# Kernel tuning notes

Measured on AMD Instinct MI355X. Metric: run time of the kernel, lower is better.

The kernel has to match this reference:

```python
import jax, jax.numpy as jnp
import numpy as np

D = 768           # input_dim == slot_dim
H, DH = 8, 64     # encoder attention heads / head dim (x-transformers defaults)
INNER = 4 * D     # ff_mult=4 GLU inner dim
EPS = 1e-8
N_ITERS = 3
SCALE = D ** -0.5


def _ln(x, g, b):
    m = jnp.mean(x, axis=-1, keepdims=True)
    v = jnp.var(x, axis=-1, keepdims=True)
    return (x - m) / jnp.sqrt(v + 1e-5) * g + b


def setup_inputs() -> dict:
    key = jax.random.key(0)
    ks = jax.random.split(key, 16)
    w = lambda i, shape, s=0.02: jax.random.normal(ks[i], shape, jnp.float32) * s
    return dict(
        x=jax.random.normal(ks[0], (32, 1024, D), jnp.float32),
        noise=jax.random.normal(ks[1], (32, 16, D), jnp.float32),
        init_mu=jax.random.normal(ks[2], (D,), jnp.float32),
        init_log_sigma=w(3, (D,), 0.05),
        Wk=w(4, (D, D)), Wv=w(5, (D, D)), Wq=w(6, (D, D)),
        ni_g=jnp.ones(D), ni_b=jnp.zeros(D),       # norm_input
        ns_g=jnp.ones(D), ns_b=jnp.zeros(D),       # norm_slots
        nica_g=jnp.ones(D), nica_b=jnp.zeros(D),   # norm_ica
        ln1_g=jnp.ones(D), ln1_b=jnp.zeros(D),     # encoder attn pre-norm
        Wq_a=w(7, (D, H * DH)), Wk_a=w(8, (D, H * DH)),
        Wv_a=w(9, (D, H * DH)), Wo_a=w(10, (H * DH, D)),
        ln2_g=jnp.ones(D), ln2_b=jnp.zeros(D),     # encoder ff pre-norm
        W1=w(11, (D, 2 * INNER)), W2=w(12, (INNER, D)),
        lnf_g=jnp.ones(D), lnf_b=jnp.zeros(D),     # encoder final norm
    )


def _inv_cross_attn(q, k, v):
    # softmax over the SLOT axis (dim i), then renormalize over keys j
    dots = jnp.einsum('bid,bjd->bij', q, k) * SCALE
    attn = jax.nn.softmax(dots, axis=1) + EPS
    attn = attn / jnp.sum(attn, axis=-1, keepdims=True)
    updates = jnp.einsum('bjd,bij->bid', v, attn)
    return updates, attn


def _encoder(h, ln1_g, ln1_b, Wq_a, Wk_a, Wv_a, Wo_a, ln2_g, ln2_b, W1, W2, lnf_g, lnf_b):
    b, n, _ = h.shape
    a = _ln(h, ln1_g, ln1_b)
    q = (a @ Wq_a).reshape(b, n, H, DH)
    k = (a @ Wk_a).reshape(b, n, H, DH)
    v = (a @ Wv_a).reshape(b, n, H, DH)
    scores = jnp.einsum('bihd,bjhd->bhij', q, k) * (DH ** -0.5)
    p = jax.nn.softmax(scores, axis=-1)
    o = jnp.einsum('bhij,bjhd->bihd', p, v).reshape(b, n, H * DH)
    h = h + o @ Wo_a
    f = _ln(h, ln2_g, ln2_b)
    u, g = jnp.split(f @ W1, 2, axis=-1)
    h = h + (u * jax.nn.silu(g)) @ W2
    return _ln(h, lnf_g, lnf_b)


def reference(x, noise, init_mu, init_log_sigma, Wk, Wv, Wq,
              ni_g, ni_b, ns_g, ns_b, nica_g, nica_b,
              ln1_g, ln1_b, Wq_a, Wk_a, Wv_a, Wo_a,
              ln2_g, ln2_b, W1, W2, lnf_g, lnf_b):
    xn = _ln(x, ni_g, ni_b)
    k = xn @ Wk
    v = xn @ Wv
    slots = init_mu + jnp.exp(init_log_sigma) * noise  # [b, n_slots, d]

    def step(slots):
        q = _ln(slots, ns_g, ns_b) @ Wq
        updates, attn = _inv_cross_attn(q, k, v)
        slots = _ln(slots + updates, nica_g, nica_b)
        slots = _encoder(slots, ln1_g, ln1_b, Wq_a, Wk_a, Wv_a, Wo_a,
                         ln2_g, ln2_b, W1, W2, lnf_g, lnf_b)
        return slots, attn

    for _ in range(N_ITERS):
        slots, _ = step(slots)
    slots, attn = step(slots)
    attn_map = jnp.transpose(attn, (0, 2, 1))  # b n hw -> b hw n
    return slots, attn_map
```

## Files before the change

kernel.cpp:

```cpp
#include <hip/hip_runtime.h>
#include <hip/hip_bf16.h>
#include <stdint.h>

typedef _Float16 f16;
typedef __attribute__((ext_vector_type(8))) _Float16 f16x8;
typedef __attribute__((ext_vector_type(4))) _Float16 f16x4;
typedef __attribute__((ext_vector_type(4))) float f32x4;

#define GLOBAL_AS __attribute__((address_space(1)))
#define LDS_AS __attribute__((address_space(3)))

#define D_DIM 768
#define NTOK 1024
#define NSLOT 16
#define NB 32
#define NTOT (NB*NTOK)
#define HDIM 512
#define INNER 3072
#define SCALE_D 0.03608439182435161f
#define SCALE_H 0.125f

template<int OUT>
__global__ __launch_bounds__(256) void mgemm64_k(
    const f16* __restrict__ A, const f16* __restrict__ Bt,
    void* __restrict__ Cout, int M, int N, int K, int Kc)
{
  __shared__ __align__(16) f16 As[64*128];
  __shared__ __align__(16) f16 Bs[64*128];
  const int tid = threadIdx.x;
  const int lane = tid & 63;
  const int wave = tid >> 6;
  const int m0 = blockIdx.x*64, n0 = blockIdx.y*64;
  const int kbeg = blockIdx.z * Kc;
  const int wm = (wave>>1)*32, wn = (wave&1)*32;
  const int quad = lane>>4, l16 = lane&15;

  const int sr = tid>>2;
  const int sc = (tid&3)*8;
  const f16* gA = A  + (size_t)(m0+sr)*K + kbeg + sc;
  const f16* gB = Bt + (size_t)(n0+sr)*K + kbeg + sc;
  LDS_AS f16* lA = (LDS_AS f16*)&As[(size_t)tid*8];
  LDS_AS f16* lB = (LDS_AS f16*)&Bs[(size_t)tid*8];

  const f16* fA0 = &As[(wm + l16)*32 + quad*8];
  const f16* fB0 = &Bs[(wn + l16)*32 + quad*8];

  f32x4 acc[2][2] = {};

  for (int k0 = 0; k0 < Kc; k0 += 128){
    #pragma unroll
    for (int p=0;p<4;++p){
      __builtin_amdgcn_global_load_lds((const GLOBAL_AS void*)(gA + k0 + p*32),
                                       (LDS_AS void*)(lA + (size_t)p*2048), 16, 0, 0);
      __builtin_amdgcn_global_load_lds((const GLOBAL_AS void*)(gB + k0 + p*32),
                                       (LDS_AS void*)(lB + (size_t)p*2048), 16, 0, 0);
    }
    __syncthreads();
    #pragma unroll
    for (int p=0;p<4;++p){
      f16x8 a0 = *(const f16x8*)(fA0 + p*2048);
      f16x8 a1 = *(const f16x8*)(fA0 + p*2048 + 16*32);
      f16x8 b0 = *(const f16x8*)(fB0 + p*2048);
      f16x8 b1 = *(const f16x8*)(fB0 + p*2048 + 16*32);
      acc[0][0] = __builtin_amdgcn_mfma_f32_16x16x32_f16(a0,b0,acc[0][0],0,0,0);
      acc[0][1] = __builtin_amdgcn_mfma_f32_16x16x32_f16(a0,b1,acc[0][1],0,0,0);
      acc[1][0] = __builtin_amdgcn_mfma_f32_16x16x32_f16(a1,b0,acc[1][0],0,0,0);
      acc[1][1] = __builtin_amdgcn_mfma_f32_16x16x32_f16(a1,b1,acc[1][1],0,0,0);
    }
    __syncthreads();
  }
  #pragma unroll
  for (int mt=0;mt<2;++mt){
    #pragma unroll
    for (int nt=0;nt<2;++nt){
      int gm = m0 + wm + mt*16 + quad*4;
      int gn = n0 + wn + nt*16 + l16;
      #pragma unroll
      for (int r=0;r<4;++r){
        float c = acc[mt][nt][r];
        size_t idx = (size_t)(gm+r)*N + gn;
        if (OUT==0)      ((float*)Cout)[idx] = c;
        else if (OUT==1) ((f16*)Cout)[idx] = (f16)c;
        else             atomicAdd(&((float*)Cout)[idx], c);
      }
    }
  }
}

__global__ __launch_bounds__(256) void w1glu_k(
    const f16* __restrict__ A, const f16* __restrict__ W1T,
    f16* __restrict__ act, int M)
{
  __shared__ __align__(16) f16 As[64*128];
  __shared__ __align__(16) f16 Bu[64*128];
  __shared__ __align__(16) f16 Bg[64*128];
  const int K = 768;
  const int tid = threadIdx.x;
  const int lane = tid & 63;
  const int wave = tid >> 6;
  const int m0 = blockIdx.x*64, n0 = blockIdx.y*64;
  const int wm = (wave>>1)*32, wn = (wave&1)*32;
  const int quad = lane>>4, l16 = lane&15;

  const int sr = tid>>2;
  const int sc = (tid&3)*8;
  const f16* gA  = A   + (size_t)(m0+sr)*K + sc;
  const f16* gBu = W1T + (size_t)(n0+sr)*K + sc;
  const f16* gBg = W1T + (size_t)(3072+n0+sr)*K + sc;
  LDS_AS f16* lA  = (LDS_AS f16*)&As[(size_t)tid*8];
  LDS_AS f16* lBu = (LDS_AS f16*)&Bu[(size_t)tid*8];
  LDS_AS f16* lBg = (LDS_AS f16*)&Bg[(size_t)tid*8];

  const f16* fA0 = &As[(wm + l16)*32 + quad*8];
  const f16* fU0 = &Bu[(wn + l16)*32 + quad*8];
  const f16* fG0 = &Bg[(wn + l16)*32 + quad*8];

  f32x4 accU[2][2] = {};
  f32x4 accG[2][2] = {};

  for (int k0 = 0; k0 < K; k0 += 128){
    #pragma unroll
    for (int p=0;p<4;++p){
      __builtin_amdgcn_global_load_lds((const GLOBAL_AS void*)(gA  + k0 + p*32),
                                       (LDS_AS void*)(lA  + (size_t)p*2048), 16, 0, 0);
      __builtin_amdgcn_global_load_lds((const GLOBAL_AS void*)(gBu + k0 + p*32),
                                       (LDS_AS void*)(lBu + (size_t)p*2048), 16, 0, 0);
      __builtin_amdgcn_global_load_lds((const GLOBAL_AS void*)(gBg + k0 + p*32),
                                       (LDS_AS void*)(lBg + (size_t)p*2048), 16, 0, 0);
    }
    __syncthreads();
    #pragma unroll
    for (int p=0;p<4;++p){
      f16x8 a0 = *(const f16x8*)(fA0 + p*2048);
      f16x8 a1 = *(const f16x8*)(fA0 + p*2048 + 16*32);
      f16x8 u0 = *(const f16x8*)(fU0 + p*2048);
      f16x8 u1 = *(const f16x8*)(fU0 + p*2048 + 16*32);
      f16x8 g0 = *(const f16x8*)(fG0 + p*2048);
      f16x8 g1 = *(const f16x8*)(fG0 + p*2048 + 16*32);
      accU[0][0] = __builtin_amdgcn_mfma_f32_16x16x32_f16(a0,u0,accU[0][0],0,0,0);
      accU[0][1] = __builtin_amdgcn_mfma_f32_16x16x32_f16(a0,u1,accU[0][1],0,0,0);
      accU[1][0] = __builtin_amdgcn_mfma_f32_16x16x32_f16(a1,u0,accU[1][0],0,0,0);
      accU[1][1] = __builtin_amdgcn_mfma_f32_16x16x32_f16(a1,u1,accU[1][1],0,0,0);
      accG[0][0] = __builtin_amdgcn_mfma_f32_16x16x32_f16(a0,g0,accG[0][0],0,0,0);
      accG[0][1] = __builtin_amdgcn_mfma_f32_16x16x32_f16(a0,g1,accG[0][1],0,0,0);
      accG[1][0] = __builtin_amdgcn_mfma_f32_16x16x32_f16(a1,g0,accG[1][0],0,0,0);
      accG[1][1] = __builtin_amdgcn_mfma_f32_16x16x32_f16(a1,g1,accG[1][1],0,0,0);
    }
    __syncthreads();
  }
  #pragma unroll
  for (int mt=0;mt<2;++mt){
    #pragma unroll
    for (int nt=0;nt<2;++nt){
      int gm = m0 + wm + mt*16 + quad*4;
      int gn = n0 + wn + nt*16 + l16;
      #pragma unroll
      for (int r=0;r<4;++r){
        float u = accU[mt][nt][r];
        float g = accG[mt][nt][r];
        float sg = g / (1.0f + __expf(-g));
        act[(size_t)(gm+r)*INNER + gn] = (f16)(u*sg);
      }
    }
  }
}

__global__ __launch_bounds__(256) void dots_k(
    const f16* __restrict__ Q,
    const f16* __restrict__ Xn,
    f16* __restrict__ attn,
    float* __restrict__ rsPart)
{
  __shared__ __align__(16) f16 qf[16*768];
  __shared__ __align__(16) f16 ks[64*128];
  __shared__ float rpart[4][16];
  const int b = blockIdx.x, jt = blockIdx.y;
  const int tid = threadIdx.x;
  const int lane = tid & 63;
  const int w = tid >> 6;
  const int quad = lane>>4, l16 = lane&15;

  #pragma unroll
  for (int c=0;c<6;++c){
    int p = c*256 + tid;
    int ki = p >> 6, qd = (p >> 4) & 3, rw = p & 15;
    f16x8 v = *(const f16x8*)(Q + ((size_t)(b*NSLOT+rw))*D_DIM + ki*32 + qd*8);
    *(f16x8*)&qf[(size_t)p*8] = v;
  }

  const f16* gK = Xn + ((size_t)(b*NTOK + jt*64 + (tid>>2)))*D_DIM + (tid&3)*8;
  LDS_AS f16* lK = (LDS_AS f16*)&ks[(size_t)tid*8];

  f32x4 acc = {};
  for (int it=0; it<6; ++it){
    #pragma unroll
    for (int p=0;p<4;++p)
      __builtin_amdgcn_global_load_lds((const GLOBAL_AS void*)(gK + it*128 + p*32),
                                       (LDS_AS void*)(lK + (size_t)p*2048), 16, 0, 0);
    __syncthreads();
    #pragma unroll
    for (int p=0;p<4;++p){
      f16x8 a  = *(const f16x8*)&qf[(((size_t)(it*4+p)*4 + quad)*16 + l16)*8];
      f16x8 bf = *(const f16x8*)&ks[(size_t)p*2048 + (w*16+l16)*32 + quad*8];
      acc = __builtin_amdgcn_mfma_f32_16x16x32_f16(a, bf, acc, 0, 0, 0);
    }
    __syncthreads();
  }

  float v0 = acc[0]*SCALE_D, v1 = acc[1]*SCALE_D, v2 = acc[2]*SCALE_D, v3 = acc[3]*SCALE_D;
  float mx = fmaxf(fmaxf(v0,v1), fmaxf(v2,v3));
  mx = fmaxf(mx, __shfl_xor(mx, 16));
  mx = fmaxf(mx, __shfl_xor(mx, 32));
  float e0 = __expf(v0-mx), e1 = __expf(v1-mx), e2 = __expf(v2-mx), e3 = __expf(v3-mx);
  float s = e0+e1+e2+e3;
  s += __shfl_xor(s, 16);
  s += __shfl_xor(s, 32);
  float inv = 1.0f/s;
  float a0 = e0*inv + 1e-8f, a1 = e1*inv + 1e-8f, a2 = e2*inv + 1e-8f, a3 = e3*inv + 1e-8f;

  int jcol = jt*64 + w*16 + l16;
  int ibase = b*NSLOT + quad*4;
  attn[(size_t)(ibase+0)*NTOK + jcol] = (f16)a0;
  attn[(size_t)(ibase+1)*NTOK + jcol] = (f16)a1;
  attn[(size_t)(ibase+2)*NTOK + jcol] = (f16)a2;
  attn[(size_t)(ibase+3)*NTOK + jcol] = (f16)a3;

  float t0=a0, t1=a1, t2=a2, t3=a3;
  #pragma unroll
  for (int m=1;m<16;m<<=1){
    t0 += __shfl_xor(t0, m);
    t1 += __shfl_xor(t1, m);
    t2 += __shfl_xor(t2, m);
    t3 += __shfl_xor(t3, m);
  }
  if (l16 == 0){
    rpart[w][quad*4+0] = t0;
    rpart[w][quad*4+1] = t1;
    rpart[w][quad*4+2] = t2;
    rpart[w][quad*4+3] = t3;
  }
  __syncthreads();
  if (tid < 16){
    float ss = rpart[0][tid] + rpart[1][tid] + rpart[2][tid] + rpart[3][tid];
    rsPart[(size_t)((b*16 + jt)<<4) + tid] = ss;
  }
}

__global__ __launch_bounds__(256) void attnv_k(
    const f16* __restrict__ attn,
    const float* __restrict__ rsPart,
    const f16* __restrict__ XnT,
    f16* __restrict__ t_out)
{
  __shared__ __align__(16) f16 Asl[16*128];
  __shared__ __align__(16) f16 Bsl[64*128];
  __shared__ float rsum[16];
  const int b = blockIdx.x, d0 = blockIdx.y*64;
  const int tid = threadIdx.x;
  const int lane = tid & 63;
  const int w = tid >> 6;
  const int quad = lane>>4, l16 = lane&15;

  if (tid < 16){
    float s = 0.f;
    #pragma unroll
    for (int jt=0;jt<16;++jt) s += rsPart[(size_t)((b*16 + jt)<<4) + tid];
    rsum[tid] = s;
  }

  const int pa = tid>>6, ta = tid&63;
  const f16* gA = attn + ((size_t)(b*NSLOT + (ta>>2)))*NTOK + pa*32 + (ta&3)*8;
  LDS_AS f16* lA = (LDS_AS f16*)&Asl[(size_t)pa*512 + ta*8];
  const f16* gB = XnT + ((size_t)(d0 + (tid>>2)))*NTOT + b*NTOK + (tid&3)*8;
  LDS_AS f16* lB = (LDS_AS f16*)&Bsl[(size_t)tid*8];

  f32x4 acc = {};
  for (int it=0; it<8; ++it){
    __builtin_amdgcn_global_load_lds((const GLOBAL_AS void*)(gA + it*128),
                                     (LDS_AS void*)lA, 16, 0, 0);
    #pragma unroll
    for (int p=0;p<4;++p)
      __builtin_amdgcn_global_load_lds((const GLOBAL_AS void*)(gB + it*128 + p*32),
                                       (LDS_AS void*)(lB + (size_t)p*2048), 16, 0, 0);
    __syncthreads();
    #pragma unroll
    for (int p=0;p<4;++p){
      f16x8 a  = *(const f16x8*)&Asl[(size_t)p*512 + l16*32 + quad*8];
      f16x8 bf = *(const f16x8*)&Bsl[(size_t)p*2048 + (w*16+l16)*32 + quad*8];
      acc = __builtin_amdgcn_mfma_f32_16x16x32_f16(a, bf, acc, 0, 0, 0);
    }
    __syncthreads();
  }
  int dcol = d0 + w*16 + l16;
  #pragma unroll
  for (int r=0;r<4;++r){
    int i = quad*4 + r;
    t_out[(size_t)(b*NSLOT + i)*D_DIM + dcol] = (f16)(acc[r] / rsum[i]);
  }
}

template<bool ADD, int OUT>
__global__ __launch_bounds__(256) void ln_k(
    const float* __restrict__ X, const float* __restrict__ X2,
    const float* __restrict__ g, const float* __restrict__ bb,
    void* __restrict__ out)
{
  __shared__ float rs[256], rss[256];
  const int row = blockIdx.x, tid = threadIdx.x;
  const float* x = X + (size_t)row*D_DIM;
  float vals[3]; float s=0.f, ss=0.f;
  #pragma unroll
  for (int t=0;t<3;++t){
    int c = tid + t*256;
    float v = x[c];
    if (ADD) v += X2[(size_t)row*D_DIM + c];
    vals[t]=v; s+=v; ss+=v*v;
  }
  rs[tid]=s; rss[tid]=ss; __syncthreads();
  for (int off=128; off>0; off>>=1){
    if (tid<off){ rs[tid]+=rs[tid+off]; rss[tid]+=rss[tid+off]; }
    __syncthreads();
  }
  float mean = rs[0]*(1.0f/768.0f);
  float var  = rss[0]*(1.0f/768.0f) - mean*mean;
  float inv  = rsqrtf(var + 1e-5f);
  #pragma unroll
  for (int t=0;t<3;++t){
    int c = tid + t*256;
    float y = (vals[t]-mean)*inv*g[c] + bb[c];
    if (OUT==1) ((f16*)out)[(size_t)row*D_DIM + c] = (f16)y;
    else        ((float*)out)[(size_t)row*D_DIM + c] = y;
  }
}

template<bool ADD>
__global__ __launch_bounds__(256) void lnln_k(
    const float* __restrict__ X, const float* __restrict__ X2,
    const float* __restrict__ g1, const float* __restrict__ b1,
    const float* __restrict__ g2, const float* __restrict__ b2,
    float* __restrict__ out1, f16* __restrict__ out2)
{
  __shared__ float rs[256], rss[256];
  const int row = blockIdx.x, tid = threadIdx.x;
  const float* x = X + (size_t)row*D_DIM;
  float vals[3]; float s=0.f, ss=0.f;
  #pragma unroll
  for (int t=0;t<3;++t){
    int c = tid + t*256;
    float v = x[c];
    if (ADD) v += X2[(size_t)row*D_DIM + c];
    vals[t]=v; s+=v; ss+=v*v;
  }
  rs[tid]=s; rss[tid]=ss; __syncthreads();
  for (int off=128; off>0; off>>=1){
    if (tid<off){ rs[tid]+=rs[tid+off]; rss[tid]+=rss[tid+off]; }
    __syncthreads();
  }
  float mean = rs[0]*(1.0f/768.0f);
  float var  = rss[0]*(1.0f/768.0f) - mean*mean;
  float inv  = rsqrtf(var + 1e-5f);
  float y[3]; float s2=0.f, ss2=0.f;
  #pragma unroll
  for (int t=0;t<3;++t){
    int c = tid + t*256;
    float yy = (vals[t]-mean)*inv*g1[c] + b1[c];
    y[t]=yy; s2+=yy; ss2+=yy*yy;
    out1[(size_t)row*D_DIM + c] = yy;
  }
  __syncthreads();
  rs[tid]=s2; rss[tid]=ss2; __syncthreads();
  for (int off=128; off>0; off>>=1){
    if (tid<off){ rs[tid]+=rs[tid+off]; rss[tid]+=rss[tid+off]; }
    __syncthreads();
  }
  float mean2 = rs[0]*(1.0f/768.0f);
  float var2  = rss[0]*(1.0f/768.0f) - mean2*mean2;
  float inv2  = rsqrtf(var2 + 1e-5f);
  #pragma unroll
  for (int t=0;t<3;++t){
    int c = tid + t*256;
    out2[(size_t)row*D_DIM + c] = (f16)((y[t]-mean2)*inv2*g2[c] + b2[c]);
  }
}

__global__ __launch_bounds__(256) void slots_init_k(
    const float* __restrict__ noise, const float* __restrict__ mu,
    const float* __restrict__ ls, float* __restrict__ slots)
{
  int idx = blockIdx.x*256 + threadIdx.x;
  int d = idx % D_DIM;
  slots[idx] = mu[d] + expf(ls[d]) * noise[idx];
}

__global__ __launch_bounds__(256) void encattn_k(
    const f16* __restrict__ QA, const f16* __restrict__ KA,
    const f16* __restrict__ VA, int QSTR,
    f16* __restrict__ O)
{
  __shared__ float qs[16][68], ks[16][68], vs[16][68], ps[16][20];
  const int b = blockIdx.x, h = blockIdx.y;
  const int tid = threadIdx.x;
  {
    int i = tid>>4, dd=(tid&15)*4;
    size_t base = ((size_t)(b*NSLOT+i))*QSTR + h*64 + dd;
    f16x4 uq = *(const f16x4*)(QA + base);
    f16x4 uk = *(const f16x4*)(KA + base);
    f16x4 uv = *(const f16x4*)(VA + base);
    float4 fq = { (float)uq.x, (float)uq.y, (float)uq.z, (float)uq.w };
    float4 fk = { (float)uk.x, (float)uk.y, (float)uk.z, (float)uk.w };
    float4 fv = { (float)uv.x, (float)uv.y, (float)uv.z, (float)uv.w };
    *(float4*)&qs[i][dd]=fq; *(float4*)&ks[i][dd]=fk; *(float4*)&vs[i][dd]=fv;
  }
  __syncthreads();
  {
    int i = tid>>4, j = tid&15;
    float s=0.f;
    #pragma unroll 8
    for (int d=0; d<64; ++d) s += qs[i][d]*ks[j][d];
    ps[i][j] = s*SCALE_H;
  }
  __syncthreads();
  if (tid < 16){
    int i = tid;
    float mx=-1e30f;
    #pragma unroll
    for (int j=0;j<16;++j) mx = fmaxf(mx, ps[i][j]);
    float sm=0.f;
    #pragma unroll
    for (int j=0;j<16;++j){ float e=__expf(ps[i][j]-mx); ps[i][j]=e; sm+=e; }
    float inv=1.0f/sm;
    #pragma unroll
    for (int j=0;j<16;++j) ps[i][j]*=inv;
  }
  __syncthreads();
  {
    int i = tid>>4, dq=(tid&15)*4;
    float a0=0,a1=0,a2=0,a3=0;
    #pragma unroll
    for (int j=0;j<16;++j){
      float p = ps[i][j];
      a0+=p*vs[j][dq+0]; a1+=p*vs[j][dq+1]; a2+=p*vs[j][dq+2]; a3+=p*vs[j][dq+3];
    }
    size_t base = ((size_t)(b*NSLOT+i))*HDIM + h*64 + dq;
    O[base+0]=(f16)a0; O[base+1]=(f16)a1; O[base+2]=(f16)a2; O[base+3]=(f16)a3;
  }
}

__global__ __launch_bounds__(256) void cast_t_k(
    const float* __restrict__ in, f16* __restrict__ out, int R, int C)
{
  __shared__ float t[32][33];
  int r0 = blockIdx.x*32, c0 = blockIdx.y*32;
  int tr = threadIdx.x & 31, g8 = threadIdx.x >> 5;
  #pragma unroll
  for (int s=0;s<4;++s){
    int r = g8*4 + s;
    t[r][tr] = in[(size_t)(r0+r)*C + c0+tr];
  }
  __syncthreads();
  #pragma unroll
  for (int s=0;s<4;++s){
    int c = g8*4+s;
    out[(size_t)(c0+c)*R + r0+tr] = (f16)t[tr][c];
  }
}

__global__ __launch_bounds__(256) void cast_k(
    const float* __restrict__ in, f16* __restrict__ out, int n)
{
  int i = blockIdx.x*256 + threadIdx.x;
  if (i < n) out[i] = (f16)in[i];
}

__global__ __launch_bounds__(256) void transp_k(
    const f16* __restrict__ in, f16* __restrict__ out, int R, int C)
{
  __shared__ f16 T[64][72];
  const int m0 = blockIdx.x*64, d0 = blockIdx.y*64;
  const int tid = threadIdx.x;
  {
    int r = tid>>2, c = (tid&3)*16;
    const f16* p = in + (size_t)(m0+r)*C + d0 + c;
    *(f16x8*)&T[r][c]   = *(const f16x8*)p;
    *(f16x8*)&T[r][c+8] = *(const f16x8*)(p+8);
  }
  __syncthreads();
  {
    int dd = tid>>2, mq = (tid&3)*16;
    f16 v[16];
    #pragma unroll
    for (int e=0;e<16;++e) v[e] = T[mq+e][dd];
    f16* p = out + (size_t)(d0+dd)*R + m0 + mq;
    *(f16x8*)p     = *(f16x8*)&v[0];
    *(f16x8*)(p+8) = *(f16x8*)&v[8];
  }
}

__global__ __launch_bounds__(256) void rsfin_k(
    const float* __restrict__ rsPart, float* __restrict__ rowsum)
{
  int idx = blockIdx.x*256 + threadIdx.x;
  if (idx < 512){
    int b = idx>>4, i = idx&15;
    float s = 0.f;
    #pragma unroll
    for (int jt=0;jt<16;++jt) s += rsPart[(size_t)((b*16+jt)<<4) + i];
    rowsum[idx] = s;
  }
}

__global__ __launch_bounds__(256) void attnout_k(
    const f16* __restrict__ attn, const float* __restrict__ rowsum,
    float* __restrict__ out)
{
  int idx = blockIdx.x*256 + threadIdx.x;
  int i = idx & 15;
  int j = (idx >> 4) & 1023;
  int b = idx >> 14;
  out[idx] = (float)attn[((size_t)b*NSLOT+i)*NTOK + j] / rowsum[b*NSLOT + i];
}

extern "C" void kernel_launch(void* const* d_in, const int* in_sizes, int n_in,
                              void* d_out, int out_size, void* d_ws, size_t ws_size,
                              hipStream_t stream) {
  const float* x        = (const float*)d_in[0];
  const float* noise    = (const float*)d_in[1];
  const float* init_mu  = (const float*)d_in[2];
  const float* init_ls  = (const float*)d_in[3];
  const float* Wk       = (const float*)d_in[4];
  const float* Wv       = (const float*)d_in[5];
  const float* Wq       = (const float*)d_in[6];
  const float* ni_g     = (const float*)d_in[7];
  const float* ni_b     = (const float*)d_in[8];
  const float* ns_g     = (const float*)d_in[9];
  const float* ns_b     = (const float*)d_in[10];
  const float* nica_g   = (const float*)d_in[11];
  const float* nica_b   = (const float*)d_in[12];
  const float* ln1_g    = (const float*)d_in[13];
  const float* ln1_b    = (const float*)d_in[14];
  const float* Wq_a     = (const float*)d_in[15];
  const float* Wk_a     = (const float*)d_in[16];
  const float* Wv_a     = (const float*)d_in[17];
  const float* Wo_a     = (const float*)d_in[18];
  const float* ln2_g    = (const float*)d_in[19];
  const float* ln2_b    = (const float*)d_in[20];
  const float* W1       = (const float*)d_in[21];
  const float* W2       = (const float*)d_in[22];
  const float* lnf_g    = (const float*)d_in[23];
  const float* lnf_b    = (const float*)d_in[24];

  char* w = (char*)d_ws;
  size_t off = 0;
  auto alloc = [&](size_t bytes)->char*{
    char* p = w + off; off += (bytes + 255) & ~(size_t)255; return p;
  };
  f16* xn_h  = (f16*)alloc((size_t)NTOT*D_DIM*2);
  f16* xnT_h = (f16*)alloc((size_t)D_DIM*NTOT*2);
  f16* Wkf   = (f16*)alloc((size_t)768*768*2);
  f16* Wqf   = (f16*)alloc((size_t)768*768*2);
  f16* BtQK  = (f16*)alloc((size_t)768*768*2);
  f16* WvT   = (f16*)alloc((size_t)768*768*2);
  f16* WqkvT = (f16*)alloc((size_t)1536*768*2);
  f16* WoaT  = (f16*)alloc((size_t)768*512*2);
  f16* W1T   = (f16*)alloc((size_t)6144*768*2);
  f16* W2T   = (f16*)alloc((size_t)768*3072*2);
  float* slots = (float*)alloc(512*768*4);
  float* hbuf  = (float*)alloc(512*768*4);
  float* upd   = (float*)alloc(512*768*4);
  f16* tmp_h  = (f16*)alloc(512*768*2);
  f16* tmp2_h = (f16*)alloc(512*768*2);
  f16* q_h    = (f16*)alloc(512*768*2);
  f16* t_h    = (f16*)alloc(512*768*2);
  f16* qkv_h  = (f16*)alloc((size_t)512*1536*2);
  f16* o_h    = (f16*)alloc(512*512*2);
  f16* act_h  = (f16*)alloc((size_t)512*3072*2);
  f16* attn_h = (f16*)alloc((size_t)NB*NSLOT*NTOK*2);
  float* rsPart = (float*)alloc((size_t)32*16*16*4);
  float* rowsum = (float*)alloc(512*4);

  auto castT = [&](const float* src, f16* dst, int R, int C){
    cast_t_k<<<dim3(R/32, C/32), 256, 0, stream>>>(src, dst, R, C);
  };
  cast_k<<<768*768/256, 256, 0, stream>>>(Wk, Wkf, 768*768);
  cast_k<<<768*768/256, 256, 0, stream>>>(Wq, Wqf, 768*768);
  castT(Wv,   WvT,             768, 768);
  castT(Wq_a, WqkvT,             768, 512);
  castT(Wk_a, WqkvT + 512*768,   768, 512);
  castT(Wv_a, WqkvT + 1024*768,  768, 512);
  castT(Wo_a, WoaT,            512, 768);
  castT(W1,   W1T,             768, 6144);
  castT(W2,   W2T,             3072, 768);

  mgemm64_k<1><<<dim3(12, 12, 1), 256, 0, stream>>>(Wkf, Wqf, BtQK, 768, 768, 768, 768);

  ln_k<false,1><<<NTOT, 256, 0, stream>>>(x, nullptr, ni_g, ni_b, xn_h);
  transp_k<<<dim3(NTOT/64, D_DIM/64), 256, 0, stream>>>(xn_h, xnT_h, NTOT, D_DIM);

  slots_init_k<<<512*768/256, 256, 0, stream>>>(noise, init_mu, init_ls, slots);
  ln_k<false,1><<<512, 256, 0, stream>>>(slots, nullptr, ns_g, ns_b, tmp2_h);

  for (int it=0; it<4; ++it){
    mgemm64_k<1><<<dim3(8, 12, 1), 256, 0, stream>>>(tmp2_h, BtQK, q_h, 512, 768, 768, 768);
    dots_k<<<dim3(NB, 16), 256, 0, stream>>>(q_h, xn_h, attn_h, rsPart);
    attnv_k<<<dim3(NB, 12), 256, 0, stream>>>(attn_h, rsPart, xnT_h, t_h);
    mgemm64_k<0><<<dim3(8, 12, 1), 256, 0, stream>>>(t_h, WvT, upd, 512, 768, 768, 768);
    lnln_k<true><<<512, 256, 0, stream>>>(slots, upd, nica_g, nica_b, ln1_g, ln1_b, hbuf, tmp_h);
    mgemm64_k<1><<<dim3(8, 24, 1), 256, 0, stream>>>(tmp_h, WqkvT, qkv_h, 512, 1536, 768, 768);
    encattn_k<<<dim3(NB, 8), 256, 0, stream>>>(qkv_h, qkv_h + 512, qkv_h + 1024, 1536, o_h);
    mgemm64_k<2><<<dim3(8, 12, 2), 256, 0, stream>>>(o_h, WoaT, hbuf, 512, 768, 512, 256);
    ln_k<false,1><<<512, 256, 0, stream>>>(hbuf, nullptr, ln2_g, ln2_b, tmp_h);
    w1glu_k<<<dim3(8, 48), 256, 0, stream>>>(tmp_h, W1T, act_h, 512);
    mgemm64_k<2><<<dim3(8, 12, 4), 256, 0, stream>>>(act_h, W2T, hbuf, 512, 768, 3072, 768);
    lnln_k<false><<<512, 256, 0, stream>>>(hbuf, nullptr, lnf_g, lnf_b, ns_g, ns_b, slots, tmp2_h);
  }

  hipMemcpyAsync(d_out, slots, (size_t)512*768*4, hipMemcpyDeviceToDevice, stream);
  rsfin_k<<<2, 256, 0, stream>>>(rsPart, rowsum);
  attnout_k<<<NB*NTOK*NSLOT/256, 256, 0, stream>>>(attn_h, rowsum, (float*)d_out + 512*768);
}
```

Measured before the change: 664.6 us.

## Fuse Wv and Wo projections into attention kernels, wave-level layernorms, merged prep

Folds the V-projection GEMM into attnv_k and the Wo projection into the encoder attention kernel, accumulating each into a residual buffer with atomics so the separate GEMMs and intermediate buffers go away. The residual buffer is pre-seeded with the slots so the slot residual add comes for free. LayerNorm kernels are rewritten to handle one row per wave using float4 loads and shuffle reductions. The weight cast and transpose launches are merged into one prep kernel, and the rowsum finalisation is folded into attnout. The atomic accumulation adds contention and makes summation order nondeterministic.

```diff
diff --git a/kernel.cpp b/kernel.cpp
--- a/kernel.cpp
+++ b/kernel.cpp
@@ -79,9 +79,8 @@
       for (int r=0;r<4;++r){
         float c = acc[mt][nt][r];
         size_t idx = (size_t)(gm+r)*N + gn;
-        if (OUT==0)      ((float*)Cout)[idx] = c;
-        else if (OUT==1) ((f16*)Cout)[idx] = (f16)c;
-        else             atomicAdd(&((float*)Cout)[idx], c);
+        if (OUT==1) ((f16*)Cout)[idx] = (f16)c;
+        else        atomicAdd(&((float*)Cout)[idx], c);
       }
     }
   }
@@ -250,11 +249,13 @@
     const f16* __restrict__ attn,
     const float* __restrict__ rsPart,
     const f16* __restrict__ XnT,
-    f16* __restrict__ t_out)
+    const f16* __restrict__ WvT,
+    float* __restrict__ accb)
 {
   __shared__ __align__(16) f16 Asl[16*128];
   __shared__ __align__(16) f16 Bsl[64*128];
   __shared__ float rsum[16];
+  __shared__ __align__(16) f16 tl[16][80];
   const int b = blockIdx.x, d0 = blockIdx.y*64;
   const int tid = threadIdx.x;
   const int lane = tid & 63;
@@ -291,113 +292,166 @@
     }
     __syncthreads();
   }
-  int dcol = d0 + w*16 + l16;
-  #pragma unroll
-  for (int r=0;r<4;++r){
-    int i = quad*4 + r;
-    t_out[(size_t)(b*NSLOT + i)*D_DIM + dcol] = (f16)(acc[r] / rsum[i]);
-  }
-}
-
-template<bool ADD, int OUT>
-__global__ __launch_bounds__(256) void ln_k(
-    const float* __restrict__ X, const float* __restrict__ X2,
+  const int dloc = w*16 + l16;
+  #pragma unroll
+  for (int r=0;r<4;++r)
+    tl[quad*4+r][dloc] = (f16)(acc[r] / rsum[quad*4+r]);
+  __syncthreads();
+  f16x8 af0 = *(const f16x8*)&tl[l16][quad*8];
+  f16x8 af1 = *(const f16x8*)&tl[l16][32 + quad*8];
+  const f16* bp = WvT + (size_t)l16*D_DIM + d0 + quad*8;
+  float* up = accb + (size_t)(b*NSLOT + quad*4)*D_DIM + l16;
+  #pragma unroll
+  for (int j=0;j<12;++j){
+    int n0 = (w*12 + j)*16;
+    f16x8 b0 = *(const f16x8*)(bp + (size_t)n0*D_DIM);
+    f16x8 b1 = *(const f16x8*)(bp + (size_t)n0*D_DIM + 32);
+    f32x4 c = {};
+    c = __builtin_amdgcn_mfma_f32_16x16x32_f16(af0, b0, c, 0,0,0);
+    c = __builtin_amdgcn_mfma_f32_16x16x32_f16(af1, b1, c, 0,0,0);
+    #pragma unroll
+    for (int r=0;r<4;++r) atomicAdd(up + (size_t)r*D_DIM + n0, c[r]);
+  }
+}
+
+__global__ __launch_bounds__(256) void lnw_k(
+    const float* __restrict__ X,
     const float* __restrict__ g, const float* __restrict__ bb,
-    void* __restrict__ out)
-{
-  __shared__ float rs[256], rss[256];
-  const int row = blockIdx.x, tid = threadIdx.x;
-  const float* x = X + (size_t)row*D_DIM;
-  float vals[3]; float s=0.f, ss=0.f;
+    f16* __restrict__ out)
+{
+  const int lane = threadIdx.x & 63;
+  const size_t row = (size_t)blockIdx.x*4 + (threadIdx.x>>6);
+  const float* x = X + row*D_DIM;
+  float4 v[3]; float s=0.f, ss=0.f;
   #pragma unroll
   for (int t=0;t<3;++t){
-    int c = tid + t*256;
-    float v = x[c];
-    if (ADD) v += X2[(size_t)row*D_DIM + c];
-    vals[t]=v; s+=v; ss+=v*v;
-  }
-  rs[tid]=s; rss[tid]=ss; __syncthreads();
-  for (int off=128; off>0; off>>=1){
-    if (tid<off){ rs[tid]+=rs[tid+off]; rss[tid]+=rss[tid+off]; }
-    __syncthreads();
-  }
-  float mean = rs[0]*(1.0f/768.0f);
-  float var  = rss[0]*(1.0f/768.0f) - mean*mean;
-  float inv  = rsqrtf(var + 1e-5f);
+    v[t] = *(const float4*)(x + lane*4 + t*256);
+    s  += v[t].x+v[t].y+v[t].z+v[t].w;
+    ss += v[t].x*v[t].x+v[t].y*v[t].y+v[t].z*v[t].z+v[t].w*v[t].w;
+  }
+  #pragma unroll
+  for (int m=1;m<64;m<<=1){ s += __shfl_xor(s,m); ss += __shfl_xor(ss,m); }
+  float mean = s*(1.0f/768.0f);
+  float inv  = rsqrtf(ss*(1.0f/768.0f) - mean*mean + 1e-5f);
   #pragma unroll
   for (int t=0;t<3;++t){
-    int c = tid + t*256;
-    float y = (vals[t]-mean)*inv*g[c] + bb[c];
-    if (OUT==1) ((f16*)out)[(size_t)row*D_DIM + c] = (f16)y;
-    else        ((float*)out)[(size_t)row*D_DIM + c] = y;
-  }
-}
-
-template<bool ADD>
-__global__ __launch_bounds__(256) void lnln_k(
-    const float* __restrict__ X, const float* __restrict__ X2,
+    int c0 = lane*4 + t*256;
+    float4 gg = *(const float4*)(g + c0);
+    float4 bv = *(const float4*)(bb + c0);
+    f16x4 h4;
+    h4.x = (f16)((v[t].x-mean)*inv*gg.x + bv.x);
+    h4.y = (f16)((v[t].y-mean)*inv*gg.y + bv.y);
+    h4.z = (f16)((v[t].z-mean)*inv*gg.z + bv.z);
+    h4.w = (f16)((v[t].w-mean)*inv*gg.w + bv.w);
+    *(f16x4*)(out + row*D_DIM + c0) = h4;
+  }
+}
+
+template<bool WACC>
+__global__ __launch_bounds__(256) void lnlnw_k(
+    const float* __restrict__ X,
     const float* __restrict__ g1, const float* __restrict__ b1,
     const float* __restrict__ g2, const float* __restrict__ b2,
-    float* __restrict__ out1, f16* __restrict__ out2)
-{
-  __shared__ float rs[256], rss[256];
-  const int row = blockIdx.x, tid = threadIdx.x;
-  const float* x = X + (size_t)row*D_DIM;
-  float vals[3]; float s=0.f, ss=0.f;
+    float* __restrict__ out1, f16* __restrict__ out2, float* __restrict__ acc)
+{
+  const int lane = threadIdx.x & 63;
+  const size_t row = (size_t)blockIdx.x*4 + (threadIdx.x>>6);
+  const float* x = X + row*D_DIM;
+  float4 v[3]; float s=0.f, ss=0.f;
   #pragma unroll
   for (int t=0;t<3;++t){
-    int c = tid + t*256;
-    float v = x[c];
-    if (ADD) v += X2[(size_t)row*D_DIM + c];
-    vals[t]=v; s+=v; ss+=v*v;
-  }
-  rs[tid]=s; rss[tid]=ss; __syncthreads();
-  for (int off=128; off>0; off>>=1){
-    if (tid<off){ rs[tid]+=rs[tid+off]; rss[tid]+=rss[tid+off]; }
-    __syncthreads();
-  }
-  float mean = rs[0]*(1.0f/768.0f);
-  float var  = rss[0]*(1.0f/768.0f) - mean*mean;
-  float inv  = rsqrtf(var + 1e-5f);
-  float y[3]; float s2=0.f, ss2=0.f;
+    v[t] = *(const float4*)(x + lane*4 + t*256);
+    s  += v[t].x+v[t].y+v[t].z+v[t].w;
+    ss += v[t].x*v[t].x+v[t].y*v[t].y+v[t].z*v[t].z+v[t].w*v[t].w;
+  }
+  #pragma unroll
+  for (int m=1;m<64;m<<=1){ s += __shfl_xor(s,m); ss += __shfl_xor(ss,m); }
+  float mean = s*(1.0f/768.0f);
+  float inv  = rsqrtf(ss*(1.0f/768.0f) - mean*mean + 1e-5f);
+  float y[3][4]; float s2=0.f, ss2=0.f;
   #pragma unroll
   for (int t=0;t<3;++t){
-    int c = tid + t*256;
-    float yy = (vals[t]-mean)*inv*g1[c] + b1[c];
-    y[t]=yy; s2+=yy; ss2+=yy*yy;
-    out1[(size_t)row*D_DIM + c] = yy;
-  }
-  __syncthreads();
-  rs[tid]=s2; rss[tid]=ss2; __syncthreads();
-  for (int off=128; off>0; off>>=1){
-    if (tid<off){ rs[tid]+=rs[tid+off]; rss[tid]+=rss[tid+off]; }
-    __syncthreads();
-  }
-  float mean2 = rs[0]*(1.0f/768.0f);
-  float var2  = rss[0]*(1.0f/768.0f) - mean2*mean2;
-  float inv2  = rsqrtf(var2 + 1e-5f);
+    int c0 = lane*4 + t*256;
+    float4 gg = *(const float4*)(g1 + c0);
+    float4 bv = *(const float4*)(b1 + c0);
+    y[t][0] = (v[t].x-mean)*inv*gg.x + bv.x;
+    y[t][1] = (v[t].y-mean)*inv*gg.y + bv.y;
+    y[t][2] = (v[t].z-mean)*inv*gg.z + bv.z;
+    y[t][3] = (v[t].w-mean)*inv*gg.w + bv.w;
+    float4 o = { y[t][0], y[t][1], y[t][2], y[t][3] };
+    *(float4*)(out1 + row*D_DIM + c0) = o;
+    if (WACC) *(float4*)(acc + row*D_DIM + c0) = o;
+    s2  += y[t][0]+y[t][1]+y[t][2]+y[t][3];
+    ss2 += y[t][0]*y[t][0]+y[t][1]*y[t][1]+y[t][2]*y[t][2]+y[t][3]*y[t][3];
+  }
+  #pragma unroll
+  for (int m=1;m<64;m<<=1){ s2 += __shfl_xor(s2,m); ss2 += __shfl_xor(ss2,m); }
+  float mean2 = s2*(1.0f/768.0f);
+  float inv2  = rsqrtf(ss2*(1.0f/768.0f) - mean2*mean2 + 1e-5f);
   #pragma unroll
   for (int t=0;t<3;++t){
-    int c = tid + t*256;
-    out2[(size_t)row*D_DIM + c] = (f16)((y[t]-mean2)*inv2*g2[c] + b2[c]);
-  }
-}
-
-__global__ __launch_bounds__(256) void slots_init_k(
+    int c0 = lane*4 + t*256;
+    float4 gg = *(const float4*)(g2 + c0);
+    float4 bv = *(const float4*)(b2 + c0);
+    f16x4 h4;
+    h4.x = (f16)((y[t][0]-mean2)*inv2*gg.x + bv.x);
+    h4.y = (f16)((y[t][1]-mean2)*inv2*gg.y + bv.y);
+    h4.z = (f16)((y[t][2]-mean2)*inv2*gg.z + bv.z);
+    h4.w = (f16)((y[t][3]-mean2)*inv2*gg.w + bv.w);
+    *(f16x4*)(out2 + row*D_DIM + c0) = h4;
+  }
+}
+
+__global__ __launch_bounds__(256) void slotsinit_k(
     const float* __restrict__ noise, const float* __restrict__ mu,
-    const float* __restrict__ ls, float* __restrict__ slots)
-{
-  int idx = blockIdx.x*256 + threadIdx.x;
-  int d = idx % D_DIM;
-  slots[idx] = mu[d] + expf(ls[d]) * noise[idx];
-}
-
-__global__ __launch_bounds__(256) void encattn_k(
+    const float* __restrict__ ls,
+    const float* __restrict__ nsg, const float* __restrict__ nsb,
+    float* __restrict__ slots, float* __restrict__ accb, f16* __restrict__ tmp2)
+{
+  const int lane = threadIdx.x & 63;
+  const size_t row = (size_t)blockIdx.x*4 + (threadIdx.x>>6);
+  float4 v[3]; float s=0.f, ss=0.f;
+  #pragma unroll
+  for (int t=0;t<3;++t){
+    int c0 = lane*4 + t*256;
+    float4 nz = *(const float4*)(noise + row*D_DIM + c0);
+    float4 m4 = *(const float4*)(mu + c0);
+    float4 l4 = *(const float4*)(ls + c0);
+    v[t].x = m4.x + __expf(l4.x)*nz.x;
+    v[t].y = m4.y + __expf(l4.y)*nz.y;
+    v[t].z = m4.z + __expf(l4.z)*nz.z;
+    v[t].w = m4.w + __expf(l4.w)*nz.w;
+    *(float4*)(slots + row*D_DIM + c0) = v[t];
+    *(float4*)(accb  + row*D_DIM + c0) = v[t];
+    s  += v[t].x+v[t].y+v[t].z+v[t].w;
+    ss += v[t].x*v[t].x+v[t].y*v[t].y+v[t].z*v[t].z+v[t].w*v[t].w;
+  }
+  #pragma unroll
+  for (int m=1;m<64;m<<=1){ s += __shfl_xor(s,m); ss += __shfl_xor(ss,m); }
+  float mean = s*(1.0f/768.0f);
+  float inv  = rsqrtf(ss*(1.0f/768.0f) - mean*mean + 1e-5f);
+  #pragma unroll
+  for (int t=0;t<3;++t){
+    int c0 = lane*4 + t*256;
+    float4 gg = *(const float4*)(nsg + c0);
+    float4 bv = *(const float4*)(nsb + c0);
+    f16x4 h4;
+    h4.x = (f16)((v[t].x-mean)*inv*gg.x + bv.x);
+    h4.y = (f16)((v[t].y-mean)*inv*gg.y + bv.y);
+    h4.z = (f16)((v[t].z-mean)*inv*gg.z + bv.z);
+    h4.w = (f16)((v[t].w-mean)*inv*gg.w + bv.w);
+    *(f16x4*)(tmp2 + row*D_DIM + c0) = h4;
+  }
+}
+
+__global__ __launch_bounds__(256) void encwo_k(
     const f16* __restrict__ QA, const f16* __restrict__ KA,
     const f16* __restrict__ VA, int QSTR,
-    f16* __restrict__ O)
+    const f16* __restrict__ WoT,
+    float* __restrict__ hb)
 {
   __shared__ float qs[16][68], ks[16][68], vs[16][68], ps[16][20];
+  __shared__ __align__(16) f16 ol[16][80];
   const int b = blockIdx.x, h = blockIdx.y;
   const int tid = threadIdx.x;
   {
@@ -441,35 +495,26 @@
       float p = ps[i][j];
       a0+=p*vs[j][dq+0]; a1+=p*vs[j][dq+1]; a2+=p*vs[j][dq+2]; a3+=p*vs[j][dq+3];
     }
-    size_t base = ((size_t)(b*NSLOT+i))*HDIM + h*64 + dq;
-    O[base+0]=(f16)a0; O[base+1]=(f16)a1; O[base+2]=(f16)a2; O[base+3]=(f16)a3;
-  }
-}
-
-__global__ __launch_bounds__(256) void cast_t_k(
-    const float* __restrict__ in, f16* __restrict__ out, int R, int C)
-{
-  __shared__ float t[32][33];
-  int r0 = blockIdx.x*32, c0 = blockIdx.y*32;
-  int tr = threadIdx.x & 31, g8 = threadIdx.x >> 5;
-  #pragma unroll
-  for (int s=0;s<4;++s){
-    int r = g8*4 + s;
-    t[r][tr] = in[(size_t)(r0+r)*C + c0+tr];
-  }
-  __syncthreads();
-  #pragma unroll
-  for (int s=0;s<4;++s){
-    int c = g8*4+s;
-    out[(size_t)(c0+c)*R + r0+tr] = (f16)t[tr][c];
-  }
-}
-
-__global__ __launch_bounds__(256) void cast_k(
-    const float* __restrict__ in, f16* __restrict__ out, int n)
-{
-  int i = blockIdx.x*256 + threadIdx.x;
-  if (i < n) out[i] = (f16)in[i];
+    f16x4 o4 = { (f16)a0, (f16)a1, (f16)a2, (f16)a3 };
+    *(f16x4*)&ol[i][dq] = o4;
+  }
+  __syncthreads();
+  const int lane = tid & 63, w = tid>>6, quad = lane>>4, l16 = lane&15;
+  f16x8 af0 = *(const f16x8*)&ol[l16][quad*8];
+  f16x8 af1 = *(const f16x8*)&ol[l16][32 + quad*8];
+  const f16* bp = WoT + (size_t)l16*HDIM + h*64 + quad*8;
+  float* hp = hb + (size_t)(b*NSLOT + quad*4)*D_DIM + l16;
+  #pragma unroll
+  for (int j=0;j<12;++j){
+    int n0 = (w*12 + j)*16;
+    f16x8 b0 = *(const f16x8*)(bp + (size_t)n0*HDIM);
+    f16x8 b1 = *(const f16x8*)(bp + (size_t)n0*HDIM + 32);
+    f32x4 c = {};
+    c = __builtin_amdgcn_mfma_f32_16x16x32_f16(af0, b0, c, 0,0,0);
+    c = __builtin_amdgcn_mfma_f32_16x16x32_f16(af1, b1, c, 0,0,0);
+    #pragma unroll
+    for (int r=0;r<4;++r) atomicAdd(hp + (size_t)r*D_DIM + n0, c[r]);
+  }
 }
 
 __global__ __launch_bounds__(256) void transp_k(
@@ -496,28 +541,70 @@
   }
 }
 
-__global__ __launch_bounds__(256) void rsfin_k(
-    const float* __restrict__ rsPart, float* __restrict__ rowsum)
-{
-  int idx = blockIdx.x*256 + threadIdx.x;
-  if (idx < 512){
-    int b = idx>>4, i = idx&15;
+__global__ __launch_bounds__(256) void prep_k(
+    const float* __restrict__ Wv,   const float* __restrict__ Wq_a,
+    const float* __restrict__ Wk_a, const float* __restrict__ Wv_a,
+    const float* __restrict__ Wo_a, const float* __restrict__ W1,
+    const float* __restrict__ W2,   const float* __restrict__ Wk,
+    const float* __restrict__ Wq,
+    f16* __restrict__ WvT, f16* __restrict__ WqkvT, f16* __restrict__ WoaT,
+    f16* __restrict__ W1T, f16* __restrict__ W2T,
+    f16* __restrict__ Wkf, f16* __restrict__ Wqf)
+{
+  __shared__ float t[32][33];
+  int bid = blockIdx.x;
+  const float* src; f16* dst; int R, C; bool tr = true;
+  if      (bid < 576)  {              src=Wv;   dst=WvT;             R=768;  C=768; }
+  else if (bid < 960)  { bid-=576;    src=Wq_a; dst=WqkvT;           R=768;  C=512; }
+  else if (bid < 1344) { bid-=960;    src=Wk_a; dst=WqkvT+512*768;   R=768;  C=512; }
+  else if (bid < 1728) { bid-=1344;   src=Wv_a; dst=WqkvT+1024*768;  R=768;  C=512; }
+  else if (bid < 2112) { bid-=1728;   src=Wo_a; dst=WoaT;            R=512;  C=768; }
+  else if (bid < 6720) { bid-=2112;   src=W1;   dst=W1T;             R=768;  C=6144; }
+  else if (bid < 9024) { bid-=6720;   src=W2;   dst=W2T;             R=3072; C=768; }
+  else if (bid < 9600) { bid-=9024;   src=Wk;   dst=Wkf;             R=768;  C=768; tr=false; }
+  else                 { bid-=9600;   src=Wq;   dst=Wqf;             R=768;  C=768; tr=false; }
+  const int tpr = C/32;
+  const int r0 = (bid / tpr)*32, c0 = (bid % tpr)*32;
+  const int lc = threadIdx.x & 31, g8 = threadIdx.x >> 5;
+  if (tr){
+    #pragma unroll
+    for (int s=0;s<4;++s){
+      int r = g8*4 + s;
+      t[r][lc] = src[(size_t)(r0+r)*C + c0+lc];
+    }
+    __syncthreads();
+    #pragma unroll
+    for (int s=0;s<4;++s){
+      int c = g8*4 + s;
+      dst[(size_t)(c0+c)*R + r0+lc] = (f16)t[lc][c];
+    }
+  } else {
+    #pragma unroll
+    for (int s=0;s<4;++s){
+      int r = g8*4 + s;
+      dst[(size_t)(r0+r)*C + c0+lc] = (f16)src[(size_t)(r0+r)*C + c0+lc];
+    }
+  }
+}
+
+__global__ __launch_bounds__(256) void attnout_k(
+    const f16* __restrict__ attn, const float* __restrict__ rsPart,
+    float* __restrict__ out)
+{
+  __shared__ float rsum[16];
+  const int bid = blockIdx.x, tid = threadIdx.x;
+  const int b = bid >> 6;
+  if (tid < 16){
     float s = 0.f;
     #pragma unroll
-    for (int jt=0;jt<16;++jt) s += rsPart[(size_t)((b*16+jt)<<4) + i];
-    rowsum[idx] = s;
-  }
-}
-
-__global__ __launch_bounds__(256) void attnout_k(
-    const f16* __restrict__ attn, const float* __restrict__ rowsum,
-    float* __restrict__ out)
-{
-  int idx = blockIdx.x*256 + threadIdx.x;
+    for (int jt=0;jt<16;++jt) s += rsPart[(size_t)((b*16+jt)<<4) + tid];
+    rsum[tid] = s;
+  }
+  __syncthreads();
+  int idx = bid*256 + tid;
   int i = idx & 15;
   int j = (idx >> 4) & 1023;
-  int b = idx >> 14;
-  out[idx] = (float)attn[((size_t)b*NSLOT+i)*NTOK + j] / rowsum[b*NSLOT + i];
+  out[idx] = (float)attn[((size_t)(b*NSLOT)+i)*NTOK + j] / rsum[i];
 }
 
 extern "C" void kernel_launch(void* const* d_in, const int* in_sizes, int n_in,
@@ -566,55 +653,42 @@
   f16* W2T   = (f16*)alloc((size_t)768*3072*2);
   float* slots = (float*)alloc(512*768*4);
   float* hbuf  = (float*)alloc(512*768*4);
-  float* upd   = (float*)alloc(512*768*4);
+  float* accb  = (float*)alloc(512*768*4);
   f16* tmp_h  = (f16*)alloc(512*768*2);
   f16* tmp2_h = (f16*)alloc(512*768*2);
   f16* q_h    = (f16*)alloc(512*768*2);
-  f16* t_h    = (f16*)alloc(512*768*2);
   f16* qkv_h  = (f16*)alloc((size_t)512*1536*2);
-  f16* o_h    = (f16*)alloc(512*512*2);
   f16* act_h  = (f16*)alloc((size_t)512*3072*2);
   f16* attn_h = (f16*)alloc((size_t)NB*NSLOT*NTOK*2);
   float* rsPart = (float*)alloc((size_t)32*16*16*4);
-  float* rowsum = (float*)alloc(512*4);
-
-  auto castT = [&](const float* src, f16* dst, int R, int C){
-    cast_t_k<<<dim3(R/32, C/32), 256, 0, stream>>>(src, dst, R, C);
-  };
-  cast_k<<<768*768/256, 256, 0, stream>>>(Wk, Wkf, 768*768);
-  cast_k<<<768*768/256, 256, 0, stream>>>(Wq, Wqf, 768*768);
-  castT(Wv,   WvT,             768, 768);
-  castT(Wq_a, WqkvT,             768, 512);
-  castT(Wk_a, WqkvT + 512*768,   768, 512);
-  castT(Wv_a, WqkvT + 1024*768,  768, 512);
-  castT(Wo_a, WoaT,            512, 768);
-  castT(W1,   W1T,             768, 6144);
-  castT(W2,   W2T,             3072, 768);
+
+  prep_k<<<10176, 256, 0, stream>>>(Wv, Wq_a, Wk_a, Wv_a, Wo_a, W1, W2, Wk, Wq,
+                                    WvT, WqkvT, WoaT, W1T, W2T, Wkf, Wqf);
 
   mgemm64_k<1><<<dim3(12, 12, 1), 256, 0, stream>>>(Wkf, Wqf, BtQK, 768, 768, 768, 768);
 
-  ln_k<false,1><<<NTOT, 256, 0, stream>>>(x, nullptr, ni_g, ni_b, xn_h);
+  lnw_k<<<NTOT/4, 256, 0, stream>>>(x, ni_g, ni_b, xn_h);
   transp_k<<<dim3(NTOT/64, D_DIM/64), 256, 0, stream>>>(xn_h, xnT_h, NTOT, D_DIM);
 
-  slots_init_k<<<512*768/256, 256, 0, stream>>>(noise, init_mu, init_ls, slots);
-  ln_k<false,1><<<512, 256, 0, stream>>>(slots, nullptr, ns_g, ns_b, tmp2_h);
+  slotsinit_k<<<128, 256, 0, stream>>>(noise, init_mu, init_ls, ns_g, ns_b,
+                                       slots, accb, tmp2_h);
 
   for (int it=0; it<4; ++it){
     mgemm64_k<1><<<dim3(8, 12, 1), 256, 0, stream>>>(tmp2_h, BtQK, q_h, 512, 768, 768, 768);
     dots_k<<<dim3(NB, 16), 256, 0, stream>>>(q_h, xn_h, attn_h, rsPart);
-    attnv_k<<<dim3(NB, 12), 256, 0, stream>>>(attn_h, rsPart, xnT_h, t_h);
-    mgemm64_k<0><<<dim3(8, 12, 1), 256, 0, stream>>>(t_h, WvT, upd, 512, 768, 768, 768);
-    lnln_k<true><<<512, 256, 0, stream>>>(slots, upd, nica_g, nica_b, ln1_g, ln1_b, hbuf, tmp_h);
+    attnv_k<<<dim3(NB, 12), 256, 0, stream>>>(attn_h, rsPart, xnT_h, WvT, accb);
+    lnlnw_k<false><<<128, 256, 0, stream>>>(accb, nica_g, nica_b, ln1_g, ln1_b,
+                                            hbuf, tmp_h, nullptr);
     mgemm64_k<1><<<dim3(8, 24, 1), 256, 0, stream>>>(tmp_h, WqkvT, qkv_h, 512, 1536, 768, 768);
-    encattn_k<<<dim3(NB, 8), 256, 0, stream>>>(qkv_h, qkv_h + 512, qkv_h + 1024, 1536, o_h);
-    mgemm64_k<2><<<dim3(8, 12, 2), 256, 0, stream>>>(o_h, WoaT, hbuf, 512, 768, 512, 256);
-    ln_k<false,1><<<512, 256, 0, stream>>>(hbuf, nullptr, ln2_g, ln2_b, tmp_h);
+    encwo_k<<<dim3(NB, 8), 256, 0, stream>>>(qkv_h, qkv_h + 512, qkv_h + 1024, 1536,
+                                             WoaT, hbuf);
+    lnw_k<<<128, 256, 0, stream>>>(hbuf, ln2_g, ln2_b, tmp_h);
     w1glu_k<<<dim3(8, 48), 256, 0, stream>>>(tmp_h, W1T, act_h, 512);
     mgemm64_k<2><<<dim3(8, 12, 4), 256, 0, stream>>>(act_h, W2T, hbuf, 512, 768, 3072, 768);
-    lnln_k<false><<<512, 256, 0, stream>>>(hbuf, nullptr, lnf_g, lnf_b, ns_g, ns_b, slots, tmp2_h);
+    lnlnw_k<true><<<128, 256, 0, stream>>>(hbuf, lnf_g, lnf_b, ns_g, ns_b,
+                                           slots, tmp2_h, accb);
   }
 
   hipMemcpyAsync(d_out, slots, (size_t)512*768*4, hipMemcpyDeviceToDevice, stream);
-  rsfin_k<<<2, 256, 0, stream>>>(rsPart, rowsum);
-  attnout_k<<<NB*NTOK*NSLOT/256, 256, 0, stream>>>(attn_h, rowsum, (float*)d_out + 512*768);
-}
+  attnout_k<<<NB*NTOK*NSLOT/256, 256, 0, stream>>>(attn_h, rsPart, (float*)d_out + 512*768);
+}
```

Measured after the change: 713.3 us. +7.3%, slower.
